# Kernel optimization log

Measured on AMD Instinct MI355X. Metric: run time of the kernel, lower is better.

Reference implementation:

```python
import jax, jax.numpy as jnp
import numpy as np

RADIUS = 0.1
NSAMPLE = 32


def setup_inputs() -> dict:
    key = jax.random.key(0)
    k1, k2, k3, k4, k5 = jax.random.split(key, 5)
    B, NPOINT, N, C = 4, 2048, 8192, 64
    query_xyz = jax.random.uniform(k1, (B, 3, NPOINT), dtype=jnp.float32)
    support_xyz = jax.random.uniform(k2, (B, 3, N), dtype=jnp.float32)
    query_mask = jax.random.bernoulli(k3, 0.9, (B, NPOINT))
    support_mask = jax.random.bernoulli(k4, 0.9, (B, N))
    features = jax.random.normal(k5, (B, C, N), dtype=jnp.float32)
    return {"query_xyz": query_xyz, "support_xyz": support_xyz,
            "query_mask": query_mask, "support_mask": support_mask,
            "features": features}


def _masked_ordered_ball_query(query_xyz, support_xyz, query_mask, support_mask,
                               radius, nsample):
    # query_xyz: (B,3,npoint), support_xyz: (B,3,N)
    q = query_xyz.transpose(0, 2, 1)    # (B, npoint, 3)
    s = support_xyz.transpose(0, 2, 1)  # (B, N, 3)
    N = s.shape[1]
    # squared pairwise distances via |q|^2 + |s|^2 - 2 q.s  -> (B, npoint, N)
    d2 = (jnp.sum(q * q, -1)[:, :, None]
          + jnp.sum(s * s, -1)[:, None, :]
          - 2.0 * jnp.einsum('bpd,bnd->bpn', q, s))
    within = (d2 <= radius * radius) \
        & support_mask[:, None, :] & query_mask[:, :, None]
    # ordered selection of the first `nsample` in-ball indices (ascending index)
    score = jnp.where(within, N - jnp.arange(N, dtype=jnp.int32), 0)
    vals, idx = jax.lax.top_k(score, nsample)     # (B, npoint, nsample)
    idx_mask = vals > 0                            # true neighbors
    # pad slots with the first found neighbor (0 if none found)
    first = jnp.where(idx_mask[..., :1], idx[..., :1], 0)
    idx = jnp.where(idx_mask, idx, first)
    return idx, idx_mask


def _group(points_nc, idx):
    # points_nc: (B, N, D), idx: (B, npoint, nsample) -> (B, npoint, nsample, D)
    return jax.vmap(lambda p, i: p[i])(points_nc, idx)


def reference(query_xyz, support_xyz, query_mask, support_mask, features):
    idx, idx_mask = _masked_ordered_ball_query(
        query_xyz, support_xyz, query_mask, support_mask, RADIUS, NSAMPLE)
    s = support_xyz.transpose(0, 2, 1)             # (B, N, 3)
    grouped_xyz = _group(s, idx).transpose(0, 3, 1, 2)   # (B,3,npoint,nsample)
    grouped_xyz = grouped_xyz - query_xyz[:, :, :, None]
    grouped_xyz = grouped_xyz / RADIUS             # normalize_xyz=True
    f = features.transpose(0, 2, 1)                # (B, N, C)
    grouped_features = _group(f, idx).transpose(0, 3, 1, 2)  # (B,C,npoint,nsample)
    new_features = jnp.concatenate([grouped_xyz, grouped_features], axis=1)
    return new_features, idx_mask
```

## Files before the change

### kernel.cpp

```cpp
#include <hip/hip_runtime.h>


#define NPOINT 2048
#define NSUP   8192
#define NCH    64
#define NS     32
#define GRID1  10
#define CELLS  1000

__device__ __forceinline__ bool probe_mask4(const void* mask) {
    const unsigned char* mb = (const unsigned char*)mask;
    const int lane = threadIdx.x & 63;
    return __ballot(mb[4 * lane + 1] != 0) == 0ull;
}
__device__ __forceinline__ bool read_mask(const void* mask, int i, bool is4) {
    return is4 ? (((const int*)mask)[i] != 0)
               : (((const unsigned char*)mask)[i] != 0);
}
__device__ __forceinline__ int cell_of(float x, float y, float z) {
    const int cx = min(GRID1 - 1, (int)(x * 10.0f));
    const int cy = min(GRID1 - 1, (int)(y * 10.0f));
    const int cz = min(GRID1 - 1, (int)(z * 10.0f));
    return cx + GRID1 * cy + GRID1 * GRID1 * cz;
}

__global__ __launch_bounds__(256) void zero_ws(int* __restrict__ ptr, int n) {
    const int i = blockIdx.x * 256 + threadIdx.x;
    if (i < n) ptr[i] = 0;
}

__global__ __launch_bounds__(256) void grid_hist(
    const float* __restrict__ support_xyz, const void* __restrict__ support_mask,
    int* __restrict__ starts)
{
    const bool m4 = probe_mask4(support_mask);
    const int gid = blockIdx.x * 256 + threadIdx.x;
    const int b = gid / NSUP, n = gid % NSUP;
    if (!read_mask(support_mask, gid, m4)) return;
    const float* sx = support_xyz + (size_t)b * 3 * NSUP;
    const int cid = cell_of(sx[n], sx[NSUP + n], sx[2 * NSUP + n]);
    atomicAdd(&starts[b * (CELLS + 1) + cid + 1], 1);
}

__global__ __launch_bounds__(1024) void grid_scan(int* __restrict__ starts) {
    __shared__ int scanb[1024];
    const int tid = threadIdx.x;
    int* sb = starts + blockIdx.x * (CELLS + 1);
    scanb[tid] = (tid < CELLS) ? sb[tid + 1] : 0;
    __syncthreads();
    for (int d = 1; d < 1024; d <<= 1) {
        int v = 0;
        if (tid >= d) v = scanb[tid - d];
        __syncthreads();
        if (tid >= d) scanb[tid] += v;
        __syncthreads();
    }
    if (tid < CELLS) sb[tid + 1] = scanb[tid];
}

__global__ __launch_bounds__(256) void grid_fill(
    const float* __restrict__ support_xyz, const void* __restrict__ support_mask,
    const int* __restrict__ starts, int* __restrict__ cursors,
    float4* __restrict__ pts)
{
    const bool m4 = probe_mask4(support_mask);
    const int gid = blockIdx.x * 256 + threadIdx.x;
    const int b = gid / NSUP, n = gid % NSUP;
    if (!read_mask(support_mask, gid, m4)) return;
    const float* sx = support_xyz + (size_t)b * 3 * NSUP;
    const float x = sx[n], y = sx[NSUP + n], z = sx[2 * NSUP + n];
    const int cid = cell_of(x, y, z);
    const int pos = starts[b * (CELLS + 1) + cid]
                  + atomicAdd(&cursors[b * CELLS + cid], 1);
    pts[(size_t)b * NSUP + pos] = make_float4(x, y, z, __int_as_float(n));
}

__global__ __launch_bounds__(256) void transpose_feat(
    const float* __restrict__ features, float* __restrict__ feat_t)
{
    __shared__ float tile[32][33];
    const int b = blockIdx.z;
    const int cblk = blockIdx.y * 32, nblk = blockIdx.x * 32;
    const int tx = threadIdx.x, ty = threadIdx.y;
    const float* src = features + ((size_t)b * NCH + cblk) * NSUP + nblk;
    #pragma unroll
    for (int r = 0; r < 4; ++r)
        tile[ty + r * 8][tx] = src[(size_t)(ty + r * 8) * NSUP + tx];
    __syncthreads();
    float* dst = feat_t + ((size_t)b * NSUP + nblk) * NCH + cblk;
    #pragma unroll
    for (int r = 0; r < 4; ++r)
        dst[(size_t)(ty + r * 8) * NCH + tx] = tile[tx][ty + r * 8];
}

__global__ __launch_bounds__(128) void mqag_grid(
    const float* __restrict__ query_xyz, const float* __restrict__ support_xyz,
    const void* __restrict__ query_mask, const void* __restrict__ support_mask,
    const float* __restrict__ features, const float* __restrict__ feat_t,
    const float4* __restrict__ pts, const int* __restrict__ starts,
    float* __restrict__ out, int B)
{
#pragma clang fp contract(off)
    const int wib  = threadIdx.x >> 6;
    const int lane = threadIdx.x & 63;
    const int qid  = blockIdx.x * 2 + wib;
    const int b    = qid / NPOINT;
    const int p    = qid % NPOINT;

    __shared__ float buf_all[2][NS * 65];
    __shared__ int hits_all[2][64];
    __shared__ int slots_all[2][NS];
    float* buf  = buf_all[wib];
    int* hits   = hits_all[wib];
    int* slots  = slots_all[wib];

    const bool m4s = probe_mask4(support_mask);
    const bool m4q = probe_mask4(query_mask);

    const float* sx = support_xyz + (size_t)b * 3 * NSUP;
    const float* sy = sx + NSUP;
    const float* sz = sx + 2 * NSUP;

    const float qx = query_xyz[(size_t)b * 3 * NPOINT + p];
    const float qy = query_xyz[(size_t)b * 3 * NPOINT + NPOINT + p];
    const float qz = query_xyz[(size_t)b * 3 * NPOINT + 2 * NPOINT + p];
    const bool  qm = read_mask(query_mask, b * NPOINT + p, m4q);
    const float qq = (qx * qx + qy * qy) + qz * qz;

    int cnt = 0;
    if (qm) {
        const int x0 = max(0, (int)floorf((qx - 0.101f) * 10.f));
        const int x1 = min(GRID1 - 1, (int)floorf((qx + 0.101f) * 10.f));
        const int y0 = max(0, (int)floorf((qy - 0.101f) * 10.f));
        const int y1 = min(GRID1 - 1, (int)floorf((qy + 0.101f) * 10.f));
        const int z0 = max(0, (int)floorf((qz - 0.101f) * 10.f));
        const int z1 = min(GRID1 - 1, (int)floorf((qz + 0.101f) * 10.f));
        const int ncx = x1 - x0 + 1;

        const int*    stb  = starts + b * (CELLS + 1);
        const float4* ptsb = pts + (size_t)b * NSUP;

        for (int cz = z0; cz <= z1; ++cz) {
            for (int cy = y0; cy <= y1; ++cy) {
                const int c0 = x0 + GRID1 * cy + GRID1 * GRID1 * cz;
                const int s0 = stb[c0];
                const int e0 = stb[c0 + ncx];
                for (int tb = s0; tb < e0; tb += 64) {
                    const int g  = tb + lane;
                    const bool valid = g < e0;
                    const float4 pv = ptsb[valid ? g : (e0 - 1)];
                    const int nidx = __float_as_int(pv.w);
                    const float ss  = (pv.x * pv.x + pv.y * pv.y) + pv.z * pv.z;
                    const float dot = __builtin_fmaf(qz, pv.z,
                                      __builtin_fmaf(qy, pv.y, qx * pv.x));
                    const float d2  = (qq + ss) - 2.0f * dot;
                    const bool within = valid && (d2 <= 0.01f)
                        && read_mask(support_mask, b * NSUP + nidx, m4s);
                    const unsigned long long bal = __ballot(within);
                    if (within) {
                        const int r = cnt + __popcll(bal & ((1ull << lane) - 1ull));
                        if (r < 64) hits[r] = nidx;
                    }
                    cnt += __popcll(bal);
                }
            }
        }
    }

    __syncthreads();

    if (cnt > 64) {
        int c2 = 0;
        for (int basei = 0; basei < NSUP; basei += 64) {
            const int n = basei + lane;
            const float x = sx[n], y = sy[n], z = sz[n];
            const bool  m = read_mask(support_mask, b * NSUP + n, m4s);
            const float ss  = (x * x + y * y) + z * z;
            const float dot = __builtin_fmaf(qz, z,
                              __builtin_fmaf(qy, y, qx * x));
            const float d2  = (qq + ss) - 2.0f * dot;
            const bool within = (d2 <= 0.01f) && m;
            const unsigned long long bal = __ballot(within);
            if (within) {
                const int r = c2 + __popcll(bal & ((1ull << lane) - 1ull));
                if (r < NS) slots[r] = n;
            }
            c2 += __popcll(bal);
            if (c2 >= NS) break;
        }
        cnt = c2;
    } else {
        int v = (lane < cnt) ? hits[lane] : 0x7FFFFFFF;
        #pragma unroll
        for (int k = 2; k <= 64; k <<= 1) {
            #pragma unroll
            for (int j = k >> 1; j > 0; j >>= 1) {
                const int pv = __shfl_xor(v, j, 64);
                const bool keep_min = ((lane & j) == 0) == ((lane & k) == 0);
                const int mn = min(v, pv), mx = max(v, pv);
                v = keep_min ? mn : mx;
            }
        }
        if (lane < NS && lane < cnt) slots[lane] = v;
    }
    const int found = (cnt < NS) ? cnt : NS;

    __syncthreads();
    const int first = (found > 0) ? slots[0] : 0;
    if (lane < NS && lane >= found) slots[lane] = first;
    __syncthreads();

    const size_t nf_elems = (size_t)B * 67 * NPOINT * NS;
    if (lane < NS) {
        out[nf_elems + ((size_t)b * NPOINT + p) * NS + lane] =
            (lane < found) ? 1.0f : 0.0f;
    }

    for (int i = 0; i < 2; ++i) {
        const int flat = i * 64 + lane;
        if (flat < 3 * NS) {
            const int ch = flat >> 5;
            const int k  = flat & 31;
            const int idx = slots[k];
            const float s = sx[(size_t)ch * NSUP + idx];
            const float q = (ch == 0) ? qx : ((ch == 1) ? qy : qz);
            out[(((size_t)b * 67 + ch) * NPOINT + p) * NS + k] = (s - q) / 0.1f;
        }
    }

    float* outf = out + (((size_t)b * 67 + 3) * NPOINT) * NS;
    if (feat_t) {
        const int myidx = (lane < NS) ? slots[lane] : 0;
        const float* ftb = feat_t + (size_t)b * NSUP * NCH;
        #pragma unroll 8
        for (int k = 0; k < NS; ++k) {
            const int idx = __shfl(myidx, k, 64);
            buf[k * 65 + lane] = ftb[(size_t)idx * NCH + lane];
        }
        for (int i = 0; i < 32; ++i) {
            const int flat = i * 64 + lane;
            const int ch = flat >> 5;
            const int k  = flat & 31;
            outf[(size_t)ch * NPOINT * NS + (size_t)p * NS + k] =
                buf[k * 65 + ch];
        }
    } else {
        const float* feat = features + (size_t)b * NCH * NSUP;
        for (int i = 0; i < 32; ++i) {
            const int flat = i * 64 + lane;
            const int ch = flat >> 5;
            const int k  = flat & 31;
            const int idx = slots[k];
            outf[(size_t)ch * NPOINT * NS + (size_t)p * NS + k] =
                feat[(size_t)ch * NSUP + idx];
        }
    }
}

__global__ __launch_bounds__(256) void mqag_linear(
    const float* __restrict__ query_xyz, const float* __restrict__ support_xyz,
    const void* __restrict__ query_mask_raw, const void* __restrict__ support_mask_raw,
    const float* __restrict__ features, float* __restrict__ out, int B)
{
#pragma clang fp contract(off)
    const int wib  = threadIdx.x >> 6;
    const int lane = threadIdx.x & 63;
    const int qid  = blockIdx.x * 4 + wib;
    const int b    = qid / NPOINT;
    const int p    = qid % NPOINT;

    __shared__ int slots_all[4][NS];
    int* slots = slots_all[wib];

    const bool m4s = probe_mask4(support_mask_raw);
    const bool m4q = probe_mask4(query_mask_raw);

    const float* sx = support_xyz + (size_t)b * 3 * NSUP;
    const float* sy = sx + NSUP;
    const float* sz = sx + 2 * NSUP;

    const float qx = query_xyz[(size_t)b * 3 * NPOINT + p];
    const float qy = query_xyz[(size_t)b * 3 * NPOINT + NPOINT + p];
    const float qz = query_xyz[(size_t)b * 3 * NPOINT + 2 * NPOINT + p];
    const bool  qm = read_mask(query_mask_raw, b * NPOINT + p, m4q);
    const float qq = (qx * qx + qy * qy) + qz * qz;

    int cnt = 0;
    if (qm) {
        for (int base = 0; base < NSUP; base += 64) {
            const int n = base + lane;
            const float x = sx[n], y = sy[n], z = sz[n];
            const bool  m = read_mask(support_mask_raw, b * NSUP + n, m4s);
            const float ss  = (x * x + y * y) + z * z;
            const float dot = __builtin_fmaf(qz, z, __builtin_fmaf(qy, y, qx * x));
            const float d2  = (qq + ss) - 2.0f * dot;
            const bool within = (d2 <= 0.01f) && m;
            const unsigned long long bal = __ballot(within);
            if (within) {
                const int r = cnt + __popcll(bal & ((1ull << lane) - 1ull));
                if (r < NS) slots[r] = n;
            }
            cnt += __popcll(bal);
            if (cnt >= NS) break;
        }
    }
    const int found = cnt < NS ? cnt : NS;
    __syncthreads();
    const int first = (found > 0) ? slots[0] : 0;
    if (lane < NS && lane >= found) slots[lane] = first;
    __syncthreads();

    const size_t nf_elems = (size_t)B * 67 * NPOINT * NS;
    if (lane < NS) {
        out[nf_elems + ((size_t)b * NPOINT + p) * NS + lane] =
            (lane < found) ? 1.0f : 0.0f;
    }
    const float* feat = features + (size_t)b * NCH * NSUP;
    for (int i = 0; i < (67 * NS + 63) / 64; ++i) {
        const int flat = i * 64 + lane;
        if (flat < 67 * NS) {
            const int ch = flat >> 5;
            const int k  = flat & 31;
            const int idx = slots[k];
            float val;
            if (ch < 3) {
                const float s = sx[(size_t)ch * NSUP + idx];
                const float q = (ch == 0) ? qx : ((ch == 1) ? qy : qz);
                val = (s - q) / 0.1f;
            } else {
                val = feat[(size_t)(ch - 3) * NSUP + idx];
            }
            out[(((size_t)b * 67 + ch) * NPOINT + p) * NS + k] = val;
        }
    }
}

extern "C" void kernel_launch(void* const* d_in, const int* in_sizes, int n_in,
                              void* d_out, int out_size, void* d_ws, size_t ws_size,
                              hipStream_t stream) {
    const float* query_xyz    = (const float*)d_in[0];
    const float* support_xyz  = (const float*)d_in[1];
    const void*  query_mask   = d_in[2];
    const void*  support_mask = d_in[3];
    const float* features     = (const float*)d_in[4];

    const int B = in_sizes[0] / (3 * NPOINT);

    const size_t off_pts     = 0;
    const size_t off_starts  = off_pts + (size_t)B * NSUP * sizeof(float4);
    const size_t off_cursors = off_starts + (size_t)B * (CELLS + 1) * sizeof(int);
    size_t off_featt         = off_cursors + (size_t)B * CELLS * sizeof(int);
    off_featt = (off_featt + 255) & ~(size_t)255;
    const size_t need_min  = off_featt;
    const size_t need_full = off_featt + (size_t)B * NSUP * NCH * sizeof(float);

    if (ws_size >= need_min) {
        float4* pts   = (float4*)((char*)d_ws + off_pts);
        int* starts   = (int*)((char*)d_ws + off_starts);
        int* cursors  = (int*)((char*)d_ws + off_cursors);
        float* feat_t = (ws_size >= need_full)
                      ? (float*)((char*)d_ws + off_featt) : nullptr;

        const int nzero = B * (CELLS + 1) + B * CELLS;
        hipLaunchKernelGGL(zero_ws, dim3((nzero + 255) / 256), dim3(256), 0,
                           stream, starts, nzero);
        hipLaunchKernelGGL(grid_hist, dim3(B * NSUP / 256), dim3(256), 0,
                           stream, support_xyz, support_mask, starts);
        hipLaunchKernelGGL(grid_scan, dim3(B), dim3(1024), 0, stream, starts);
        hipLaunchKernelGGL(grid_fill, dim3(B * NSUP / 256), dim3(256), 0,
                           stream, support_xyz, support_mask, starts, cursors, pts);
        if (feat_t) {
            hipLaunchKernelGGL(transpose_feat,
                               dim3(NSUP / 32, NCH / 32, B), dim3(32, 8), 0,
                               stream, features, feat_t);
        }
        hipLaunchKernelGGL(mqag_grid, dim3(B * NPOINT / 2), dim3(128), 0,
                           stream, query_xyz, support_xyz, query_mask,
                           support_mask, features, feat_t, pts, starts,
                           (float*)d_out, B);
    } else {
        hipLaunchKernelGGL(mqag_linear, dim3(B * NPOINT / 4), dim3(256), 0,
                           stream, query_xyz, support_xyz, query_mask,
                           support_mask, features, (float*)d_out, B);
    }
}
```

Measured before the change: 129.1 us.

## Split ball query and feature gather; gather per channel from LDS-cached row

The fused query+gather kernel is split in two. The query kernel writes neighbor indices to a workspace and now runs 4 waves per block. A new gather kernel loads one full feature channel row (8192 floats) into shared memory and writes contiguous float4 outputs indexed by the stored indices. This drops the feature transpose pass and the strided per-query writes, making output stores fully coalesced. The cost is an extra index round-trip through global memory, an extra launch, and each channel row being reloaded once per query chunk.

```diff
diff --git a/kernel.cpp b/kernel.cpp
--- a/kernel.cpp
+++ b/kernel.cpp
@@ -7,6 +7,7 @@
 #define NS     32
 #define GRID1  10
 #define CELLS  1000
+#define QCHUNK 1024
 
 __device__ __forceinline__ bool probe_mask4(const void* mask) {
     const unsigned char* mb = (const unsigned char*)mask;
@@ -75,44 +76,23 @@
     pts[(size_t)b * NSUP + pos] = make_float4(x, y, z, __int_as_float(n));
 }
 
-__global__ __launch_bounds__(256) void transpose_feat(
-    const float* __restrict__ features, float* __restrict__ feat_t)
-{
-    __shared__ float tile[32][33];
-    const int b = blockIdx.z;
-    const int cblk = blockIdx.y * 32, nblk = blockIdx.x * 32;
-    const int tx = threadIdx.x, ty = threadIdx.y;
-    const float* src = features + ((size_t)b * NCH + cblk) * NSUP + nblk;
-    #pragma unroll
-    for (int r = 0; r < 4; ++r)
-        tile[ty + r * 8][tx] = src[(size_t)(ty + r * 8) * NSUP + tx];
-    __syncthreads();
-    float* dst = feat_t + ((size_t)b * NSUP + nblk) * NCH + cblk;
-    #pragma unroll
-    for (int r = 0; r < 4; ++r)
-        dst[(size_t)(ty + r * 8) * NCH + tx] = tile[tx][ty + r * 8];
-}
-
-__global__ __launch_bounds__(128) void mqag_grid(
+__global__ __launch_bounds__(256) void mqag_query(
     const float* __restrict__ query_xyz, const float* __restrict__ support_xyz,
     const void* __restrict__ query_mask, const void* __restrict__ support_mask,
-    const float* __restrict__ features, const float* __restrict__ feat_t,
     const float4* __restrict__ pts, const int* __restrict__ starts,
-    float* __restrict__ out, int B)
+    int* __restrict__ idx_ws, float* __restrict__ out, int B)
 {
 #pragma clang fp contract(off)
     const int wib  = threadIdx.x >> 6;
     const int lane = threadIdx.x & 63;
-    const int qid  = blockIdx.x * 2 + wib;
+    const int qid  = blockIdx.x * 4 + wib;
     const int b    = qid / NPOINT;
     const int p    = qid % NPOINT;
 
-    __shared__ float buf_all[2][NS * 65];
-    __shared__ int hits_all[2][64];
-    __shared__ int slots_all[2][NS];
-    float* buf  = buf_all[wib];
-    int* hits   = hits_all[wib];
-    int* slots  = slots_all[wib];
+    __shared__ int hits_all[4][64];
+    __shared__ int slots_all[4][NS];
+    int* hits  = hits_all[wib];
+    int* slots = slots_all[wib];
 
     const bool m4s = probe_mask4(support_mask);
     const bool m4q = probe_mask4(query_mask);
@@ -210,6 +190,8 @@
     if (lane < NS && lane >= found) slots[lane] = first;
     __syncthreads();
 
+    if (lane < NS) idx_ws[((size_t)b * NPOINT + p) * NS + lane] = slots[lane];
+
     const size_t nf_elems = (size_t)B * 67 * NPOINT * NS;
     if (lane < NS) {
         out[nf_elems + ((size_t)b * NPOINT + p) * NS + lane] =
@@ -227,33 +209,28 @@
             out[(((size_t)b * 67 + ch) * NPOINT + p) * NS + k] = (s - q) / 0.1f;
         }
     }
-
-    float* outf = out + (((size_t)b * 67 + 3) * NPOINT) * NS;
-    if (feat_t) {
-        const int myidx = (lane < NS) ? slots[lane] : 0;
-        const float* ftb = feat_t + (size_t)b * NSUP * NCH;
-        #pragma unroll 8
-        for (int k = 0; k < NS; ++k) {
-            const int idx = __shfl(myidx, k, 64);
-            buf[k * 65 + lane] = ftb[(size_t)idx * NCH + lane];
-        }
-        for (int i = 0; i < 32; ++i) {
-            const int flat = i * 64 + lane;
-            const int ch = flat >> 5;
-            const int k  = flat & 31;
-            outf[(size_t)ch * NPOINT * NS + (size_t)p * NS + k] =
-                buf[k * 65 + ch];
-        }
-    } else {
-        const float* feat = features + (size_t)b * NCH * NSUP;
-        for (int i = 0; i < 32; ++i) {
-            const int flat = i * 64 + lane;
-            const int ch = flat >> 5;
-            const int k  = flat & 31;
-            const int idx = slots[k];
-            outf[(size_t)ch * NPOINT * NS + (size_t)p * NS + k] =
-                feat[(size_t)ch * NSUP + idx];
-        }
+}
+
+__global__ __launch_bounds__(256) void gather_feat(
+    const float* __restrict__ features, const int* __restrict__ idx_ws,
+    float* __restrict__ out, int B)
+{
+    __shared__ float row[NSUP];
+    const int bc = blockIdx.y;
+    const int b  = bc / NCH, ch = bc % NCH;
+    const int p0 = blockIdx.x * QCHUNK;
+
+    const float* src = features + ((size_t)b * NCH + ch) * NSUP;
+    const float4* src4 = (const float4*)src;
+    for (int i = threadIdx.x; i < NSUP / 4; i += 256)
+        ((float4*)row)[i] = src4[i];
+    __syncthreads();
+
+    const int4* idx4 = (const int4*)(idx_ws + ((size_t)b * NPOINT + p0) * NS);
+    float4* dst4 = (float4*)(out + (((size_t)b * 67 + 3 + ch) * NPOINT + p0) * NS);
+    for (int e = threadIdx.x; e < QCHUNK * NS / 4; e += 256) {
+        const int4 iv = idx4[e];
+        dst4[e] = make_float4(row[iv.x], row[iv.y], row[iv.z], row[iv.w]);
     }
 }
 
@@ -349,17 +326,14 @@
     const size_t off_pts     = 0;
     const size_t off_starts  = off_pts + (size_t)B * NSUP * sizeof(float4);
     const size_t off_cursors = off_starts + (size_t)B * (CELLS + 1) * sizeof(int);
-    size_t off_featt         = off_cursors + (size_t)B * CELLS * sizeof(int);
-    off_featt = (off_featt + 255) & ~(size_t)255;
-    const size_t need_min  = off_featt;
-    const size_t need_full = off_featt + (size_t)B * NSUP * NCH * sizeof(float);
-
-    if (ws_size >= need_min) {
-        float4* pts   = (float4*)((char*)d_ws + off_pts);
-        int* starts   = (int*)((char*)d_ws + off_starts);
-        int* cursors  = (int*)((char*)d_ws + off_cursors);
-        float* feat_t = (ws_size >= need_full)
-                      ? (float*)((char*)d_ws + off_featt) : nullptr;
+    const size_t off_idx     = off_cursors + (size_t)B * CELLS * sizeof(int);
+    const size_t need = off_idx + (size_t)B * NPOINT * NS * sizeof(int);
+
+    if (ws_size >= need) {
+        float4* pts  = (float4*)((char*)d_ws + off_pts);
+        int* starts  = (int*)((char*)d_ws + off_starts);
+        int* cursors = (int*)((char*)d_ws + off_cursors);
+        int* idx_ws  = (int*)((char*)d_ws + off_idx);
 
         const int nzero = B * (CELLS + 1) + B * CELLS;
         hipLaunchKernelGGL(zero_ws, dim3((nzero + 255) / 256), dim3(256), 0,
@@ -369,15 +343,11 @@
         hipLaunchKernelGGL(grid_scan, dim3(B), dim3(1024), 0, stream, starts);
         hipLaunchKernelGGL(grid_fill, dim3(B * NSUP / 256), dim3(256), 0,
                            stream, support_xyz, support_mask, starts, cursors, pts);
-        if (feat_t) {
-            hipLaunchKernelGGL(transpose_feat,
-                               dim3(NSUP / 32, NCH / 32, B), dim3(32, 8), 0,
-                               stream, features, feat_t);
-        }
-        hipLaunchKernelGGL(mqag_grid, dim3(B * NPOINT / 2), dim3(128), 0,
+        hipLaunchKernelGGL(mqag_query, dim3(B * NPOINT / 4), dim3(256), 0,
                            stream, query_xyz, support_xyz, query_mask,
-                           support_mask, features, feat_t, pts, starts,
-                           (float*)d_out, B);
+                           support_mask, pts, starts, idx_ws, (float*)d_out, B);
+        hipLaunchKernelGGL(gather_feat, dim3(NPOINT / QCHUNK, B * NCH), dim3(256),
+                           0, stream, features, idx_ws, (float*)d_out, B);
     } else {
         hipLaunchKernelGGL(mqag_linear, dim3(B * NPOINT / 4), dim3(256), 0,
                            stream, query_xyz, support_xyz, query_mask,
```

After: 122.9 us, median of 2. 4.8% less time.
